# Optimization experiments

Measured on AMD Instinct MI355X. Metric: run time of the kernel, lower is better.

## Reference

```python
import jax, jax.numpy as jnp
import numpy as np

B, N, C, C_OUT, LAYERS, ORDER = 512, 207, 207, 512, 2, 2
EPS = 1e-5


def setup_inputs() -> dict:
    key = jax.random.key(0)
    ks = jax.random.split(key, 12)
    C3 = (ORDER * 1 + 1) * C  # support_len=1 (adaptive only), order=2 -> 3*C
    inp = {
        "x": jax.random.normal(ks[0], (B, N, C), dtype=jnp.float32),
        "nodevec1": jax.random.normal(ks[1], (N, 10), dtype=jnp.float32),
        "nodevec2": jax.random.normal(ks[2], (10, N), dtype=jnp.float32),
        # per-layer gcn 1x1 conv: (layers, C_out=C, C_in=3C) + bias
        "Wg": jax.random.normal(ks[3], (LAYERS, C, C3), dtype=jnp.float32) * (1.0 / np.sqrt(C3)),
        "bg": jax.random.normal(ks[4], (LAYERS, C), dtype=jnp.float32) * 0.01,
        # per-layer BatchNorm1d (eval mode) params over channel dim C
        "gamma": 1.0 + 0.1 * jax.random.normal(ks[5], (LAYERS, C), dtype=jnp.float32),
        "beta": 0.1 * jax.random.normal(ks[6], (LAYERS, C), dtype=jnp.float32),
        "rmean": 0.1 * jax.random.normal(ks[7], (LAYERS, C), dtype=jnp.float32),
        "rvar": jax.random.uniform(ks[8], (LAYERS, C), dtype=jnp.float32, minval=0.5, maxval=1.5),
        # final Conv1d(C, C_OUT, k=1)
        "Wm": jax.random.normal(ks[9], (C_OUT, C), dtype=jnp.float32) * (1.0 / np.sqrt(C)),
        "bm": jax.random.normal(ks[10], (C_OUT,), dtype=jnp.float32) * 0.01,
    }
    return inp


def reference(x, nodevec1, nodevec2, Wg, bg, gamma, beta, rmean, rvar, Wm, bm):
    # x: (B, N, C) -> (B, C, N)
    h = jnp.transpose(x, (0, 2, 1))
    # adaptive adjacency: softmax(relu(E1 @ E2), axis=1), shape (N, N)
    adp = jax.nn.softmax(jax.nn.relu(nodevec1 @ nodevec2), axis=1)
    for i in range(LAYERS):
        # diffusion conv: out[b,c,w] = sum_v h[b,c,v] * A[w,v]  (einsum 'ncvl,nwv->ncwl')
        x1 = jnp.einsum('bcv,wv->bcw', h, adp)
        x2 = jnp.einsum('bcv,wv->bcw', x1, adp)
        cat = jnp.concatenate([h, x1, x2], axis=1)  # (B, 3C, N)
        # 1x1 conv (linear over channels) + bias
        g = jnp.einsum('bcn,oc->bon', cat, Wg[i]) + bg[i][None, :, None]
        # BatchNorm1d in eval mode (dropout is identity at inference)
        inv = gamma[i] / jnp.sqrt(rvar[i] + EPS)
        h = g * inv[None, :, None] + (beta[i] - rmean[i] * inv)[None, :, None]
    # final Conv1d 1x1: C -> C_OUT
    out = jnp.einsum('bcn,oc->bon', h, Wm) + bm[None, :, None]  # (B, C_OUT, N)
    return jnp.transpose(out, (0, 2, 1))  # (B, N, C_OUT)
```

## Files before the change

kernel.cpp:

```cpp
#include <hip/hip_runtime.h>
#include <hip/hip_bf16.h>

#define B 512
#define N 207
#define C 207
#define CO 512
#define NLAYERS 2
#define EPS 1e-5f

#define STRIDE 224
#define ROWS 208
#define KSTEPS 7
#define RS ((size_t)ROWS*STRIDE)
#define XSTR 232

typedef unsigned short ushort;
typedef short s8v __attribute__((ext_vector_type(8)));
typedef float f4 __attribute__((ext_vector_type(4)));
typedef unsigned short u16x4 __attribute__((ext_vector_type(4)));

__device__ __forceinline__ ushort f2bu(float f) {
    __hip_bfloat16 h = __float2bfloat16(f);
    return __builtin_bit_cast(ushort, h);
}
__device__ __forceinline__ float bu2f(ushort u) {
    union { unsigned int u; float f; } v; v.u = ((unsigned int)u) << 16;
    return v.f;
}
__device__ __forceinline__ u16x4 packbf4(f4 v) {
    u16x4 r;
    #pragma unroll
    for (int i = 0; i < 4; ++i) r[i] = f2bu(v[i]);
    return r;
}

__device__ __forceinline__ s8v gload16(const ushort* p) {
    s8v v;
    asm volatile("global_load_dwordx4 %0, %1, off"
                 : "=v"(v) : "v"(p) : "memory");
    return v;
}

#define WAIT_VM(n) asm volatile("s_waitcnt vmcnt(" #n ")" ::: "memory")
#define WAIT_LGKM0 asm volatile("s_waitcnt lgkmcnt(0)" ::: "memory")

__global__ void adp_kernel(const float* __restrict__ nv1, const float* __restrict__ nv2,
                           ushort* __restrict__ P1) {
    int w = blockIdx.x, j = threadIdx.x;
    __shared__ float red[256];
    if (w >= 207) {
        if (j < STRIDE) P1[w*STRIDE + j] = 0;
        return;
    }
    float val = 0.f;
    if (j < 207) {
        float acc = 0.f;
        #pragma unroll
        for (int k = 0; k < 10; ++k) acc += nv1[w*10 + k] * nv2[k*207 + j];
        val = fmaxf(acc, 0.f);
    }
    red[j] = (j < 207) ? val : -1e30f;
    __syncthreads();
    for (int off = 128; off > 0; off >>= 1) {
        if (j < off) red[j] = fmaxf(red[j], red[j+off]);
        __syncthreads();
    }
    float m = red[0];
    __syncthreads();
    float e = (j < 207) ? expf(val - m) : 0.f;
    red[j] = e;
    __syncthreads();
    for (int off = 128; off > 0; off >>= 1) {
        if (j < off) red[j] += red[j+off];
        __syncthreads();
    }
    float inv = 1.f / red[0];
    if (j < STRIDE) P1[w*STRIDE + j] = f2bu(e * inv);
}

__global__ void p2_kernel(const ushort* __restrict__ P1, ushort* __restrict__ P2) {
    int v = blockIdx.x*16 + threadIdx.x;
    int w = blockIdx.y*16 + threadIdx.y;
    if (w < STRIDE && v < STRIDE) {
        float acc = 0.f;
        for (int u = 0; u < 207; ++u) acc += bu2f(P1[w*STRIDE + u]) * bu2f(P1[u*STRIDE + v]);
        P2[w*STRIDE + v] = f2bu(acc);
    }
}

__global__ void bn_kernel(const float* __restrict__ gamma, const float* __restrict__ beta,
                          const float* __restrict__ rmean, const float* __restrict__ rvar,
                          const float* __restrict__ bg,
                          float* __restrict__ binv, float* __restrict__ bfold) {
    int i = blockIdx.x*256 + threadIdx.x;
    if (i >= NLAYERS*ROWS) return;
    int l = i / ROWS, o = i % ROWS;
    float iv = 0.f, bf = 0.f;
    if (o < 207) {
        float g = gamma[l*207 + o];
        iv = g * rsqrtf(rvar[l*207 + o] + EPS);
        bf = bg[l*207 + o]*iv + beta[l*207 + o] - rmean[l*207 + o]*iv;
    }
    binv[i] = iv; bfold[i] = bf;
}

__global__ void wg_prep(const float* __restrict__ Wg, ushort* __restrict__ Wgp) {
    int idx = blockIdx.x*256 + threadIdx.x;
    if (idx >= NLAYERS*3*ROWS*STRIDE) return;
    int k = idx % STRIDE;
    int o = (idx / STRIDE) % ROWS;
    int seg = (idx / (STRIDE*ROWS)) % 3;
    int l = idx / (STRIDE*ROWS*3);
    float v = (o < 207 && k < 207) ? Wg[((size_t)(l*207 + o))*621 + seg*207 + k] : 0.f;
    Wgp[idx] = f2bu(v);
}

__global__ void wm_prep(const float* __restrict__ Wm, ushort* __restrict__ Wmp) {
    int idx = blockIdx.x*256 + threadIdx.x;
    if (idx >= CO*STRIDE) return;
    int k = idx % STRIDE, o = idx / STRIDE;
    Wmp[idx] = f2bu(k < 207 ? Wm[o*207 + k] : 0.f);
}

__global__ void h0_kernel(const float* __restrict__ x, ushort* __restrict__ Hcv,
                          ushort* __restrict__ Hnc) {
    __shared__ float t[32][33];
    int b = blockIdx.z;
    int n0 = blockIdx.x*32, c0 = blockIdx.y*32;
    int tx = threadIdx.x, ty = threadIdx.y;
    for (int i = ty; i < 32; i += 8) {
        int n = n0 + i, c = c0 + tx;
        t[i][tx] = (n < 207 && c < 207) ? x[((size_t)b*207 + n)*207 + c] : 0.f;
    }
    __syncthreads();
    size_t base = (size_t)b*RS;
    for (int i = ty; i < 32; i += 8) {
        int n = n0 + i, c = c0 + tx;
        if (n < ROWS && c < STRIDE) Hnc[base + (size_t)n*STRIDE + c] = f2bu(t[i][tx]);
    }
    for (int i = ty; i < 32; i += 8) {
        int c = c0 + i, n = n0 + tx;
        if (c < ROWS && n < STRIDE) Hcv[base + (size_t)c*STRIDE + n] = f2bu(t[tx][i]);
    }
}

template<int ROUNDS_>
__device__ __forceinline__ void stage512(ushort* __restrict__ tile,
                                         const ushort* __restrict__ src,
                                         int rbase, int rmax, int kbase, int tid) {
    int lane = tid & 63, wave = tid >> 6;
    int chunk = ((lane & 3) ^ ((lane >> 3) & 3)) * 8;
    #pragma unroll
    for (int i = 0; i < ROUNDS_; ++i) {
        int r = rbase + i*128 + wave*16 + (lane >> 2);
        r = (r > rmax) ? rmax : r;
        const ushort* g = src + (size_t)r*STRIDE + kbase + chunk;
        ushort* l = tile + i*4096 + wave*512;
        __builtin_amdgcn_global_load_lds(
            (const __attribute__((address_space(1))) void*)g,
            (__attribute__((address_space(3))) void*)l, 16, 0, 0);
    }
}

__global__ __launch_bounds__(512, 2)
void layer_kernel(const ushort* __restrict__ Hcv, const ushort* __restrict__ Hnc,
                  const ushort* __restrict__ P1, const ushort* __restrict__ P2,
                  const ushort* __restrict__ Wgl,
                  const float* __restrict__ bi, const float* __restrict__ bsh,
                  ushort* __restrict__ Hcv_out, ushort* __restrict__ Hnc_out) {
    __shared__ __align__(16) ushort lds[59392];
    ushort* A1t = lds;
    ushort* A2t = lds + 8192;
    ushort* Bt  = lds + 16384;
    ushort* X1l = lds;
    ushort* X2l = lds + 29696;

    int tile = blockIdx.x;
    int b = blockIdx.y;
    int n0 = tile*128;
    size_t boff = (size_t)b*RS;
    const ushort* Hcvb = Hcv + boff;
    const ushort* Hncb = Hnc + boff;

    int tid = threadIdx.x, lane = tid & 63, wid = tid >> 6;
    int frow = lane & 15;
    int fko   = (lane >> 4)*8;
    int fko_s = (((lane >> 4) ^ ((lane >> 1) & 3)))*8;
    int g4 = (lane >> 4)*4;

    int wmA = wid >> 1, wnA = wid & 1;
    f4 aX1[2][8], aX2[2][8];
    #pragma unroll
    for (int i = 0; i < 2; ++i)
        #pragma unroll
        for (int j = 0; j < 8; ++j) { aX1[i][j] = (f4)0.f; aX2[i][j] = (f4)0.f; }

    stage512<1>(A1t, P1, n0, 223, 0, tid);
    stage512<1>(A2t, P2, n0, 223, 0, tid);
    stage512<2>(Bt,  Hcvb, 0, 207, 0, tid);

    for (int ks = 0; ks < KSTEPS; ++ks) {
        int cur = ks & 1;
        if (ks + 1 < KSTEPS) {
            int k1 = (ks + 1)*32;
            stage512<1>(A1t + (cur^1)*4096, P1, n0, 223, k1, tid);
            stage512<1>(A2t + (cur^1)*4096, P2, n0, 223, k1, tid);
            stage512<2>(Bt  + (cur^1)*8192, Hcvb, 0, 207, k1, tid);
            WAIT_VM(4);
        } else {
            WAIT_VM(0);
        }
        __builtin_amdgcn_s_barrier();
        s8v a1[2], a2[2], bfr[8];
        #pragma unroll
        for (int f = 0; f < 2; ++f) {
            a1[f] = *(const s8v*)&A1t[cur*4096 + (wmA*32 + f*16 + frow)*32 + fko_s];
            a2[f] = *(const s8v*)&A2t[cur*4096 + (wmA*32 + f*16 + frow)*32 + fko_s];
        }
        #pragma unroll
        for (int f = 0; f < 8; ++f)
            bfr[f] = *(const s8v*)&Bt[cur*8192 + (wnA*128 + f*16 + frow)*32 + fko_s];
        #pragma unroll
        for (int fm = 0; fm < 2; ++fm)
            #pragma unroll
            for (int fn = 0; fn < 8; ++fn) {
                aX1[fm][fn] = __builtin_amdgcn_mfma_f32_16x16x32_bf16(bfr[fn], a1[fm], aX1[fm][fn], 0, 0, 0);
                aX2[fm][fn] = __builtin_amdgcn_mfma_f32_16x16x32_bf16(bfr[fn], a2[fm], aX2[fm][fn], 0, 0, 0);
            }
        WAIT_LGKM0;
        __builtin_amdgcn_s_barrier();
    }
    #pragma unroll
    for (int fm = 0; fm < 2; ++fm) {
        int w = wmA*32 + fm*16 + (lane & 15);
        #pragma unroll
        for (int fn = 0; fn < 8; ++fn) {
            int cq = wnA*128 + fn*16 + g4;
            if (cq < STRIDE) {
                *(u16x4*)&X1l[w*XSTR + cq] = packbf4(aX1[fm][fn]);
                *(u16x4*)&X2l[w*XSTR + cq] = packbf4(aX2[fm][fn]);
            }
        }
    }
    WAIT_LGKM0;
    __builtin_amdgcn_s_barrier();

    int wmB = wid >> 1, wnB = wid & 1;
    f4 aG[4][4];
    #pragma unroll
    for (int i = 0; i < 4; ++i)
        #pragma unroll
        for (int j = 0; j < 4; ++j) aG[i][j] = (f4)0.f;

    const ushort* wseg[3] = { Wgl, Wgl + RS, Wgl + 2*RS };
    size_t woff[4];
    #pragma unroll
    for (int f = 0; f < 4; ++f) {
        int o = wmB*64 + f*16 + frow;
        if (o > 207) o = 207;
        woff[f] = (size_t)o*STRIDE + fko;
    }
    const ushort* hptr[4];
    #pragma unroll
    for (int f = 0; f < 4; ++f) {
        int n = n0 + wnB*64 + f*16 + frow;
        if (n > 207) n = 207;
        hptr[f] = Hncb + (size_t)n*STRIDE + fko;
    }

    s8v wbuf[2][4], hbuf[2][4];
    #pragma unroll
    for (int f = 0; f < 4; ++f)
        wbuf[0][f] = gload16(wseg[1] + woff[f]);

    #pragma unroll
    for (int ks = 0; ks < 21; ++ks) {
        const int seg = (ks < 7) ? 1 : (ks < 14) ? 2 : 0;
        const int k0  = (ks % 7)*32;
        if (ks + 1 < 21) {
            const int seg1 = (ks+1 < 7) ? 1 : (ks+1 < 14) ? 2 : 0;
            const int k01  = ((ks+1) % 7)*32;
            #pragma unroll
            for (int f = 0; f < 4; ++f)
                wbuf[(ks+1)&1][f] = gload16(wseg[seg1] + woff[f] + k01);
            if (seg1 == 0) {
                #pragma unroll
                for (int f = 0; f < 4; ++f)
                    hbuf[(ks+1)&1][f] = gload16(hptr[f] + k01);
            }
        }
        if (ks == 20)      { WAIT_VM(0); }
        else if (ks >= 13) { WAIT_VM(8); }
        else               { WAIT_VM(4); }
        __builtin_amdgcn_sched_barrier(0);

        s8v bfr[4];
        if (seg == 0) {
            #pragma unroll
            for (int fn = 0; fn < 4; ++fn) bfr[fn] = hbuf[ks&1][fn];
        } else {
            const ushort* Xs = (seg == 1) ? X1l : X2l;
            #pragma unroll
            for (int fn = 0; fn < 4; ++fn)
                bfr[fn] = *(const s8v*)&Xs[(wnB*64 + fn*16 + frow)*XSTR + k0 + fko];
        }
        #pragma unroll
        for (int fm = 0; fm < 4; ++fm)
            #pragma unroll
            for (int fn = 0; fn < 4; ++fn)
                aG[fm][fn] = __builtin_amdgcn_mfma_f32_16x16x32_bf16(bfr[fn], wbuf[ks&1][fm], aG[fm][fn], 0, 0, 0);
    }

    ushort* Ocv = Hcv_out + boff;
    ushort* Onc = Hnc_out + boff;
    #pragma unroll
    for (int fm = 0; fm < 4; ++fm) {
        int o = wmB*64 + fm*16 + (lane & 15);
        if (o >= ROWS) continue;
        float iv = bi[o], sh = bsh[o];
        #pragma unroll
        for (int fn = 0; fn < 4; ++fn) {
            int nq = n0 + wnB*64 + fn*16 + g4;
            if (nq >= STRIDE) continue;
            f4 h = aG[fm][fn]*iv + sh;
            u16x4 hq = packbf4(h);
            *(u16x4*)(Ocv + (size_t)o*STRIDE + nq) = hq;
            #pragma unroll
            for (int r = 0; r < 4; ++r) {
                int n = nq + r;
                if (n < ROWS) Onc[(size_t)n*STRIDE + o] = hq[r];
            }
        }
    }
}

__global__ __launch_bounds__(512, 2)
void final_kernel(const ushort* __restrict__ Hnc, const ushort* __restrict__ Wmp,
                  const float* __restrict__ bm, float* __restrict__ out) {
    __shared__ __align__(16) ushort At[2][128*32], Bt[2][512*32];
    int b = blockIdx.y;
    int n0 = blockIdx.x*128;
    const ushort* Hb = Hnc + (size_t)b*RS;
    int tid = threadIdx.x, lane = tid & 63, wid = tid >> 6;
    int wo = wid >> 1, wn = wid & 1;
    int frow = lane & 15;
    int fko_s = (((lane >> 4) ^ ((lane >> 1) & 3)))*8;

    f4 acc[4][8];
    #pragma unroll
    for (int i = 0; i < 4; ++i)
        #pragma unroll
        for (int j = 0; j < 8; ++j) acc[i][j] = (f4)0.f;

    stage512<1>(At[0], Hb,  n0, 207, 0, tid);
    stage512<4>(Bt[0], Wmp, 0, 511, 0, tid);

    for (int ks = 0; ks < KSTEPS; ++ks) {
        int cur = ks & 1;
        if (ks + 1 < KSTEPS) {
            int k1 = (ks + 1)*32;
            stage512<1>(At[cur^1], Hb,  n0, 207, k1, tid);
            stage512<4>(Bt[cur^1], Wmp, 0, 511, k1, tid);
            WAIT_VM(5);
        } else {
            WAIT_VM(0);
        }
        __builtin_amdgcn_s_barrier();
        s8v a[4], bf[8];
        #pragma unroll
        for (int f = 0; f < 4; ++f)
            a[f]  = *(const s8v*)&At[cur][(wn*64 + f*16 + frow)*32 + fko_s];
        #pragma unroll
        for (int f = 0; f < 8; ++f)
            bf[f] = *(const s8v*)&Bt[cur][(wo*128 + f*16 + frow)*32 + fko_s];
        #pragma unroll
        for (int fm = 0; fm < 4; ++fm)
            #pragma unroll
            for (int fn = 0; fn < 8; ++fn)
                acc[fm][fn] = __builtin_amdgcn_mfma_f32_16x16x32_bf16(bf[fn], a[fm], acc[fm][fn], 0, 0, 0);
        WAIT_LGKM0;
        __builtin_amdgcn_s_barrier();
    }

    int g4 = (lane >> 4)*4;
    #pragma unroll
    for (int fm = 0; fm < 4; ++fm) {
        int n = n0 + wn*64 + fm*16 + (lane & 15);
        if (n >= 207) continue;
        float* orow = out + ((size_t)b*207 + n)*CO;
        #pragma unroll
        for (int fn = 0; fn < 8; ++fn) {
            int oq = wo*128 + fn*16 + g4;
            f4 bias = *(const f4*)(bm + oq);
            f4 v = acc[fm][fn] + bias;
            *(f4*)(orow + oq) = v;
        }
    }
}

static inline size_t align_up(size_t v, size_t a) { return (v + a - 1) & ~(a - 1); }

extern "C" void kernel_launch(void* const* d_in, const int* in_sizes, int n_in,
                              void* d_out, int out_size, void* d_ws, size_t ws_size,
                              hipStream_t stream) {
    const float* x     = (const float*)d_in[0];
    const float* nv1   = (const float*)d_in[1];
    const float* nv2   = (const float*)d_in[2];
    const float* Wg    = (const float*)d_in[3];
    const float* bg    = (const float*)d_in[4];
    const float* gamma = (const float*)d_in[5];
    const float* beta  = (const float*)d_in[6];
    const float* rmean = (const float*)d_in[7];
    const float* rvar  = (const float*)d_in[8];
    const float* Wm    = (const float*)d_in[9];
    const float* bm    = (const float*)d_in[10];
    float* out = (float*)d_out;

    char* ws = (char*)d_ws;
    const size_t bufN = (size_t)B*RS*sizeof(ushort);
    ushort* P1   = (ushort*)ws; ws += align_up((size_t)STRIDE*STRIDE*2, 512);
    ushort* P2   = (ushort*)ws; ws += align_up((size_t)STRIDE*STRIDE*2, 512);
    float* binv  = (float*)ws;  ws += align_up((size_t)NLAYERS*ROWS*4, 512);
    float* bfold = (float*)ws;  ws += align_up((size_t)NLAYERS*ROWS*4, 512);
    ushort* Wgp  = (ushort*)ws; ws += align_up((size_t)NLAYERS*3*RS*2, 512);
    ushort* Wmp  = (ushort*)ws; ws += align_up((size_t)CO*STRIDE*2, 512);
    ushort* A0 = (ushort*)ws; ws += align_up(bufN, 512);
    ushort* A1 = (ushort*)ws; ws += align_up(bufN, 512);
    ushort* B0 = (ushort*)ws; ws += align_up(bufN, 512);
    ushort* B1 = (ushort*)ws; ws += align_up(bufN, 512);

    adp_kernel<<<STRIDE, 256, 0, stream>>>(nv1, nv2, P1);
    p2_kernel<<<dim3(14, 14), dim3(16, 16), 0, stream>>>(P1, P2);
    bn_kernel<<<(NLAYERS*ROWS + 255)/256, 256, 0, stream>>>(gamma, beta, rmean, rvar, bg, binv, bfold);
    wg_prep<<<(NLAYERS*3*ROWS*STRIDE + 255)/256, 256, 0, stream>>>(Wg, Wgp);
    wm_prep<<<(CO*STRIDE + 255)/256, 256, 0, stream>>>(Wm, Wmp);
    h0_kernel<<<dim3(7, 7, B), dim3(32, 8), 0, stream>>>(x, A0, A1);

    layer_kernel<<<dim3(2, B), 512, 0, stream>>>(A0, A1, P1, P2,
        Wgp, binv, bfold, B0, B1);
    layer_kernel<<<dim3(2, B), 512, 0, stream>>>(B0, B1, P1, P2,
        Wgp + (size_t)3*RS, binv + ROWS, bfold + ROWS, A0, A1);

    final_kernel<<<dim3(2, B), 512, 0, stream>>>(A1, Wmp, bm, out);
}
```

Before: 391.6 us.

## Shrink layer kernel node tile to 64 for higher occupancy

Cuts the per-block node slab of the layer kernel from 128 to 64 and doubles the grid. The wave layout is reorganised (4x2 for diffusion, 8x1 over output channels for the 1x1 conv), the A1/A2 staging is merged into one routine, and LDS drops to about half so four blocks can fit per CU. Global loads now use a scalar base plus a 32-bit vector offset to save registers. The cost is that every block restages the full H tile and all of Wg for half as many nodes, roughly doubling that redundant traffic.

```diff
diff --git a/kernel.cpp b/kernel.cpp
--- a/kernel.cpp
+++ b/kernel.cpp
@@ -13,6 +13,7 @@
 #define KSTEPS 7
 #define RS ((size_t)ROWS*STRIDE)
 #define XSTR 232
+#define SLAB 64
 
 typedef unsigned short ushort;
 typedef short s8v __attribute__((ext_vector_type(8)));
@@ -34,10 +35,10 @@
     return r;
 }
 
-__device__ __forceinline__ s8v gload16(const ushort* p) {
+__device__ __forceinline__ s8v gload16s(const ushort* base, unsigned off) {
     s8v v;
-    asm volatile("global_load_dwordx4 %0, %1, off"
-                 : "=v"(v) : "v"(p) : "memory");
+    asm volatile("global_load_dwordx4 %0, %1, %2"
+                 : "=v"(v) : "v"(off), "s"(base) : "memory");
     return v;
 }
 
@@ -162,22 +163,36 @@
     }
 }
 
-__global__ __launch_bounds__(512, 2)
+__device__ __forceinline__ void stageA(ushort* __restrict__ tile,
+                                       const ushort* __restrict__ P1,
+                                       const ushort* __restrict__ P2,
+                                       int rbase, int kbase, int tid) {
+    int lane = tid & 63, wave = tid >> 6;
+    const ushort* src = (wave < 4) ? P1 : P2;
+    int chunk = ((lane & 3) ^ ((lane >> 3) & 3)) * 8;
+    int r = rbase + (wave & 3)*16 + (lane >> 2);
+    r = (r > 223) ? 223 : r;
+    const ushort* g = src + (size_t)r*STRIDE + kbase + chunk;
+    ushort* l = tile + (wave >> 2)*2048 + (wave & 3)*512;
+    __builtin_amdgcn_global_load_lds(
+        (const __attribute__((address_space(1))) void*)g,
+        (__attribute__((address_space(3))) void*)l, 16, 0, 0);
+}
+
+__global__ __launch_bounds__(512, 4)
 void layer_kernel(const ushort* __restrict__ Hcv, const ushort* __restrict__ Hnc,
                   const ushort* __restrict__ P1, const ushort* __restrict__ P2,
                   const ushort* __restrict__ Wgl,
                   const float* __restrict__ bi, const float* __restrict__ bsh,
                   ushort* __restrict__ Hcv_out, ushort* __restrict__ Hnc_out) {
-    __shared__ __align__(16) ushort lds[59392];
-    ushort* A1t = lds;
-    ushort* A2t = lds + 8192;
-    ushort* Bt  = lds + 16384;
-    ushort* X1l = lds;
-    ushort* X2l = lds + 29696;
-
-    int tile = blockIdx.x;
+    __shared__ __align__(16) ushort lds[29696];
+    ushort* Abuf = lds;
+    ushort* Bbuf = lds + 8192;
+    ushort* X1l  = lds;
+    ushort* X2l  = lds + 14848;
+
+    int n0 = blockIdx.x * SLAB;
     int b = blockIdx.y;
-    int n0 = tile*128;
     size_t boff = (size_t)b*RS;
     const ushort* Hcvb = Hcv + boff;
     const ushort* Hncb = Hnc + boff;
@@ -188,54 +203,54 @@
     int fko_s = (((lane >> 4) ^ ((lane >> 1) & 3)))*8;
     int g4 = (lane >> 4)*4;
 
-    int wmA = wid >> 1, wnA = wid & 1;
-    f4 aX1[2][8], aX2[2][8];
+    int wmA = wid >> 2, wnA = wid & 3;
+    f4 aX1[2][4], aX2[2][4];
     #pragma unroll
     for (int i = 0; i < 2; ++i)
         #pragma unroll
-        for (int j = 0; j < 8; ++j) { aX1[i][j] = (f4)0.f; aX2[i][j] = (f4)0.f; }
-
-    stage512<1>(A1t, P1, n0, 223, 0, tid);
-    stage512<1>(A2t, P2, n0, 223, 0, tid);
-    stage512<2>(Bt,  Hcvb, 0, 207, 0, tid);
-
+        for (int j = 0; j < 4; ++j) { aX1[i][j] = (f4)0.f; aX2[i][j] = (f4)0.f; }
+
+    stageA(Abuf, P1, P2, n0, 0, tid);
+    stage512<2>(Bbuf, Hcvb, 0, 207, 0, tid);
+
+    #pragma unroll
     for (int ks = 0; ks < KSTEPS; ++ks) {
         int cur = ks & 1;
         if (ks + 1 < KSTEPS) {
             int k1 = (ks + 1)*32;
-            stage512<1>(A1t + (cur^1)*4096, P1, n0, 223, k1, tid);
-            stage512<1>(A2t + (cur^1)*4096, P2, n0, 223, k1, tid);
-            stage512<2>(Bt  + (cur^1)*8192, Hcvb, 0, 207, k1, tid);
-            WAIT_VM(4);
+            stageA(Abuf + (cur^1)*4096, P1, P2, n0, k1, tid);
+            stage512<2>(Bbuf + (cur^1)*8192, Hcvb, 0, 207, k1, tid);
+            WAIT_VM(3);
         } else {
             WAIT_VM(0);
         }
         __builtin_amdgcn_s_barrier();
-        s8v a1[2], a2[2], bfr[8];
+        s8v a1[2], a2[2], bfr[4];
         #pragma unroll
         for (int f = 0; f < 2; ++f) {
-            a1[f] = *(const s8v*)&A1t[cur*4096 + (wmA*32 + f*16 + frow)*32 + fko_s];
-            a2[f] = *(const s8v*)&A2t[cur*4096 + (wmA*32 + f*16 + frow)*32 + fko_s];
-        }
-        #pragma unroll
-        for (int f = 0; f < 8; ++f)
-            bfr[f] = *(const s8v*)&Bt[cur*8192 + (wnA*128 + f*16 + frow)*32 + fko_s];
+            a1[f] = *(const s8v*)&Abuf[cur*4096 + (wmA*32 + f*16 + frow)*32 + fko_s];
+            a2[f] = *(const s8v*)&Abuf[cur*4096 + 2048 + (wmA*32 + f*16 + frow)*32 + fko_s];
+        }
+        #pragma unroll
+        for (int f = 0; f < 4; ++f)
+            bfr[f] = *(const s8v*)&Bbuf[cur*8192 + (wnA*64 + f*16 + frow)*32 + fko_s];
         #pragma unroll
         for (int fm = 0; fm < 2; ++fm)
             #pragma unroll
-            for (int fn = 0; fn < 8; ++fn) {
+            for (int fn = 0; fn < 4; ++fn) {
                 aX1[fm][fn] = __builtin_amdgcn_mfma_f32_16x16x32_bf16(bfr[fn], a1[fm], aX1[fm][fn], 0, 0, 0);
                 aX2[fm][fn] = __builtin_amdgcn_mfma_f32_16x16x32_bf16(bfr[fn], a2[fm], aX2[fm][fn], 0, 0, 0);
             }
         WAIT_LGKM0;
         __builtin_amdgcn_s_barrier();
     }
+
     #pragma unroll
     for (int fm = 0; fm < 2; ++fm) {
         int w = wmA*32 + fm*16 + (lane & 15);
         #pragma unroll
-        for (int fn = 0; fn < 8; ++fn) {
-            int cq = wnA*128 + fn*16 + g4;
+        for (int fn = 0; fn < 4; ++fn) {
+            int cq = wnA*64 + fn*16 + g4;
             if (cq < STRIDE) {
                 *(u16x4*)&X1l[w*XSTR + cq] = packbf4(aX1[fm][fn]);
                 *(u16x4*)&X2l[w*XSTR + cq] = packbf4(aX2[fm][fn]);
@@ -245,33 +260,30 @@
     WAIT_LGKM0;
     __builtin_amdgcn_s_barrier();
 
-    int wmB = wid >> 1, wnB = wid & 1;
-    f4 aG[4][4];
-    #pragma unroll
-    for (int i = 0; i < 4; ++i)
+    unsigned woffB[2], hoffB[4];
+    #pragma unroll
+    for (int f = 0; f < 2; ++f) {
+        int o = wid*32 + f*16 + frow;
+        if (o > 207) o = 207;
+        woffB[f] = (unsigned)((o*STRIDE + fko)*2);
+    }
+    #pragma unroll
+    for (int f = 0; f < 4; ++f) {
+        int n = n0 + f*16 + frow;
+        if (n > 207) n = 207;
+        hoffB[f] = (unsigned)((n*STRIDE + fko)*2);
+    }
+
+    f4 aG[2][4];
+    #pragma unroll
+    for (int i = 0; i < 2; ++i)
         #pragma unroll
         for (int j = 0; j < 4; ++j) aG[i][j] = (f4)0.f;
 
-    const ushort* wseg[3] = { Wgl, Wgl + RS, Wgl + 2*RS };
-    size_t woff[4];
-    #pragma unroll
-    for (int f = 0; f < 4; ++f) {
-        int o = wmB*64 + f*16 + frow;
-        if (o > 207) o = 207;
-        woff[f] = (size_t)o*STRIDE + fko;
-    }
-    const ushort* hptr[4];
-    #pragma unroll
-    for (int f = 0; f < 4; ++f) {
-        int n = n0 + wnB*64 + f*16 + frow;
-        if (n > 207) n = 207;
-        hptr[f] = Hncb + (size_t)n*STRIDE + fko;
-    }
-
-    s8v wbuf[2][4], hbuf[2][4];
-    #pragma unroll
-    for (int f = 0; f < 4; ++f)
-        wbuf[0][f] = gload16(wseg[1] + woff[f]);
+    s8v wbuf[2][2], hbuf[2][4];
+    #pragma unroll
+    for (int f = 0; f < 2; ++f)
+        wbuf[0][f] = gload16s(Wgl + RS, woffB[f]);
 
     #pragma unroll
     for (int ks = 0; ks < 21; ++ks) {
@@ -279,19 +291,20 @@
         const int k0  = (ks % 7)*32;
         if (ks + 1 < 21) {
             const int seg1 = (ks+1 < 7) ? 1 : (ks+1 < 14) ? 2 : 0;
-            const int k01  = ((ks+1) % 7)*32;
-            #pragma unroll
-            for (int f = 0; f < 4; ++f)
-                wbuf[(ks+1)&1][f] = gload16(wseg[seg1] + woff[f] + k01);
+            const unsigned k01b = (unsigned)(((ks+1) % 7)*64);
+            const ushort* wsegp = Wgl + (size_t)seg1*RS;
+            #pragma unroll
+            for (int f = 0; f < 2; ++f)
+                wbuf[(ks+1)&1][f] = gload16s(wsegp, woffB[f] + k01b);
             if (seg1 == 0) {
                 #pragma unroll
                 for (int f = 0; f < 4; ++f)
-                    hbuf[(ks+1)&1][f] = gload16(hptr[f] + k01);
+                    hbuf[(ks+1)&1][f] = gload16s(Hncb, hoffB[f] + k01b);
             }
         }
         if (ks == 20)      { WAIT_VM(0); }
-        else if (ks >= 13) { WAIT_VM(8); }
-        else               { WAIT_VM(4); }
+        else if (ks >= 13) { WAIT_VM(6); }
+        else               { WAIT_VM(2); }
         __builtin_amdgcn_sched_barrier(0);
 
         s8v bfr[4];
@@ -302,10 +315,10 @@
             const ushort* Xs = (seg == 1) ? X1l : X2l;
             #pragma unroll
             for (int fn = 0; fn < 4; ++fn)
-                bfr[fn] = *(const s8v*)&Xs[(wnB*64 + fn*16 + frow)*XSTR + k0 + fko];
-        }
-        #pragma unroll
-        for (int fm = 0; fm < 4; ++fm)
+                bfr[fn] = *(const s8v*)&Xs[(fn*16 + frow)*XSTR + k0 + fko];
+        }
+        #pragma unroll
+        for (int fm = 0; fm < 2; ++fm)
             #pragma unroll
             for (int fn = 0; fn < 4; ++fn)
                 aG[fm][fn] = __builtin_amdgcn_mfma_f32_16x16x32_bf16(bfr[fn], wbuf[ks&1][fm], aG[fm][fn], 0, 0, 0);
@@ -314,13 +327,13 @@
     ushort* Ocv = Hcv_out + boff;
     ushort* Onc = Hnc_out + boff;
     #pragma unroll
-    for (int fm = 0; fm < 4; ++fm) {
-        int o = wmB*64 + fm*16 + (lane & 15);
+    for (int fm = 0; fm < 2; ++fm) {
+        int o = wid*32 + fm*16 + (lane & 15);
         if (o >= ROWS) continue;
         float iv = bi[o], sh = bsh[o];
         #pragma unroll
         for (int fn = 0; fn < 4; ++fn) {
-            int nq = n0 + wnB*64 + fn*16 + g4;
+            int nq = n0 + fn*16 + g4;
             if (nq >= STRIDE) continue;
             f4 h = aG[fm][fn]*iv + sh;
             u16x4 hq = packbf4(h);
@@ -436,9 +449,9 @@
     wm_prep<<<(CO*STRIDE + 255)/256, 256, 0, stream>>>(Wm, Wmp);
     h0_kernel<<<dim3(7, 7, B), dim3(32, 8), 0, stream>>>(x, A0, A1);
 
-    layer_kernel<<<dim3(2, B), 512, 0, stream>>>(A0, A1, P1, P2,
+    layer_kernel<<<dim3(4, B), 512, 0, stream>>>(A0, A1, P1, P2,
         Wgp, binv, bfold, B0, B1);
-    layer_kernel<<<dim3(2, B), 512, 0, stream>>>(B0, B1, P1, P2,
+    layer_kernel<<<dim3(4, B), 512, 0, stream>>>(B0, B1, P1, P2,
         Wgp + (size_t)3*RS, binv + ROWS, bfold + ROWS, A0, A1);
 
     final_kernel<<<dim3(2, B), 512, 0, stream>>>(A1, Wmp, bm, out);
```

Measured after the change: 412.8 us. +5.4%, slower.
